# Kernel tuning notes

Hardware: AMD Instinct MI355X
Metric: run time of the kernel (lower is better)

Reference implementation:

```python
import jax, jax.numpy as jnp
import numpy as np

N = 100000
E = 1600000
BN_EPS = 1e-5


def setup_inputs() -> dict:
    key = jax.random.key(0)
    ks = jax.random.split(key, 32)
    rn = lambda k, shape, s=0.05: jax.random.normal(k, shape, jnp.float32) * s
    inp = {
        "x": jax.random.normal(ks[0], (N, 2), jnp.float32),
        "edge_index": jax.random.randint(ks[1], (2, E), 0, N, dtype=jnp.int64),
        # GIN conv1 mlp: Linear(1,256) -> BN(256) -> ReLU -> Linear(256,128)
        "w1": rn(ks[2], (1, 256)), "b1": rn(ks[3], (256,)),
        "g1": jax.random.uniform(ks[4], (256,), jnp.float32, 0.5, 1.5),
        "be1": rn(ks[5], (256,)),
        "m1": rn(ks[6], (256,)),
        "v1": jax.random.uniform(ks[7], (256,), jnp.float32, 0.5, 1.5),
        "w2": rn(ks[8], (256, 128)), "b2": rn(ks[9], (128,)),
        # GIN conv2 mlp: Linear(128,64) -> BN(64) -> ReLU -> Linear(64,64)
        "w3": rn(ks[10], (128, 64)), "b3": rn(ks[11], (64,)),
        "g2": jax.random.uniform(ks[12], (64,), jnp.float32, 0.5, 1.5),
        "be2": rn(ks[13], (64,)),
        "m2": rn(ks[14], (64,)),
        "v2": jax.random.uniform(ks[15], (64,), jnp.float32, 0.5, 1.5),
        # Bilinear(64, 64, 96)
        "wb": rn(ks[16], (96, 64, 64)), "bb": rn(ks[17], (96,)),
        # linear3: 96 -> 6
        "w5": rn(ks[18], (96, 6)), "b5": rn(ks[19], (6,)),
        # linear2: 6 -> 6
        "w6": rn(ks[20], (6, 6)), "b6": rn(ks[21], (6,)),
    }
    return inp


def reference(x, edge_index, w1, b1, g1, be1, m1, v1, w2, b2,
              w3, b3, g2, be2, m2, v2, w4_unused=None, wb=None, bb=None,
              w5=None, b5=None, w6=None, b6=None):
    # note: kept signature explicit below; see _reference
    raise NotImplementedError


def _bn(h, g, b, m, v):
    # inference-mode batchnorm with running stats
    return (h - m) * jax.lax.rsqrt(v + BN_EPS) * g + b


def reference(x, edge_index, w1, b1, g1, be1, m1, v1, w2, b2,
              w3, b3, g2, be2, m2, v2, wb, bb, w5, b5, w6, b6):
    src, dst = edge_index[0], edge_index[1]
    n = x.shape[0]

    def agg(h):
        # GIN sum aggregation: (1+eps)*x + sum_{j in N(i)} x_j, eps=0
        return h + jax.ops.segment_sum(h[src], dst, num_segments=n)

    def block(col):  # col: [n, 1]
        h = agg(col)
        h = jnp.maximum(_bn(h @ w1 + b1, g1, be1, m1, v1), 0.0) @ w2 + b2  # [n,128]
        h = agg(h)
        h = jnp.maximum(_bn(h @ w3 + b3, g2, be2, m2, v2), 0.0)            # mlp2 ends with BN+ReLU? no:
        return h

    # mlp2 = Linear(128,64)->BN(64)->ReLU->Linear(64,64); rebuild correctly inline:
    def block2(col):
        h = agg(col)
        h = jnp.maximum(_bn(h @ w1 + b1, g1, be1, m1, v1), 0.0) @ w2 + b2  # [n,128]
        h = agg(h)
        h = jnp.maximum(_bn(h @ w3 + b3, g2, be2, m2, v2), 0.0)
        return h

    h1 = block2(x[:, 1:2])  # column tmp-1 = 1 first
    h2 = block2(x[:, 0:1])  # then column 0
    # mlp2's final Linear(64,64) is folded below? No -- apply final linear of mlp2:
    # (handled in block2 already via w3 only; second linear uses separate weights)
    hb = jnp.einsum('ni,kij,nj->nk', h1, wb, h2) + bb  # Bilinear(64,64,96)
    h = jnp.maximum(hb @ w5 + b5, 0.0)                 # relu(linear3)
    h = h @ w6 + b6                                    # linear2
    return jax.nn.log_softmax(h, axis=1)
```

## Files before the change

### kernel.cpp

```cpp
#include <hip/hip_runtime.h>
#include <hip/hip_bf16.h>

#define NN 100000
#define NE 1600000
#define EPS 1e-5f
#define NCHUNK 98
#define NB 196
#define BCAP2 10240
#define RND 4096
#define NRND 391

typedef __attribute__((ext_vector_type(8))) short short8;
typedef __attribute__((ext_vector_type(4))) float f32x4;

__device__ __forceinline__ float b2f_lo(unsigned u){ return __uint_as_float(u << 16); }
__device__ __forceinline__ float b2f_hi(unsigned u){ return __uint_as_float(u & 0xffff0000u); }
__device__ __forceinline__ float b2f_u(unsigned short u){ return __uint_as_float(((unsigned)u) << 16); }
__device__ __forceinline__ unsigned short f2b(float f){
  __hip_bfloat16 h = __float2bfloat16(f);
  return __builtin_bit_cast(unsigned short, h);
}

__global__ void k_probe(const int* __restrict__ ei32, int* __restrict__ flag, int* __restrict__ gcur){
  __shared__ int cnt;
  if (threadIdx.x == 0) cnt = 0;
  __syncthreads();
  if (ei32[threadIdx.x * 2 + 1] == 0) atomicAdd(&cnt, 1);
  __syncthreads();
  if (threadIdx.x == 0) flag[0] = (cnt > 200) ? 1 : 0;
  for (int i = threadIdx.x; i < NB; i += 256) gcur[i] = i * BCAP2;
}

__global__ __launch_bounds__(1024) void k_bin(const void* __restrict__ ei, const int* __restrict__ flag,
                                              int* __restrict__ gcur, int* __restrict__ staged){
  __shared__ int hcnt[256];
  __shared__ int pref[256];
  __shared__ int bnd[200];
  __shared__ int hrun[196];
  __shared__ int gb[196];
  __shared__ int sbuf[RND];
  int t = threadIdx.x;
  int base = blockIdx.x * RND;
  bool f64 = (flag[0] != 0);
  int pay[4], bkt[4];
  #pragma unroll
  for (int k = 0; k < 4; ++k){
    int e = base + k * 1024 + t;
    if (e < NE){
      int src, dst;
      if (f64){ src = (int)((const long long*)ei)[e]; dst = (int)((const long long*)ei)[NE + e]; }
      else    { src = ((const int*)ei)[e];            dst = ((const int*)ei)[NE + e]; }
      pay[k] = (src << 9) | (dst & 511);
      bkt[k] = dst >> 9;
    } else { pay[k] = 0; bkt[k] = -1; }
  }
  if (t < 256) hcnt[t] = 0;
  __syncthreads();
  #pragma unroll
  for (int k = 0; k < 4; ++k)
    if (bkt[k] >= 0) atomicAdd(&hcnt[bkt[k]], 1);
  __syncthreads();
  if (t < 256) pref[t] = hcnt[t];
  __syncthreads();
  for (int off = 1; off < 256; off <<= 1){
    int v = 0;
    if (t < 256 && t >= off) v = pref[t - off];
    __syncthreads();
    if (t < 256) pref[t] += v;
    __syncthreads();
  }
  if (t < 196){
    int excl = pref[t] - hcnt[t];
    bnd[t] = excl;
    hrun[t] = excl;
    gb[t] = (hcnt[t] > 0) ? atomicAdd(&gcur[t], hcnt[t]) : 0;
  }
  if (t == 196) bnd[196] = 0;
  __syncthreads();
  if (t == 0) bnd[196] = pref[255];
  __syncthreads();
  #pragma unroll
  for (int k = 0; k < 4; ++k)
    if (bkt[k] >= 0){
      int lp = atomicAdd(&hrun[bkt[k]], 1);
      sbuf[lp] = pay[k];
    }
  __syncthreads();
  int total = bnd[196];
  for (int i = t; i < total; i += 1024){
    int b = 0;
    #pragma unroll
    for (int sh = 128; sh > 0; sh >>= 1)
      if (b + sh <= 196 && bnd[b + sh] <= i) b += sh;
    staged[gb[b] + (i - bnd[b])] = sbuf[i];
  }
}

__global__ __launch_bounds__(256) void k_bdeg(const int* __restrict__ staged, const int* __restrict__ gcur,
                                              int* __restrict__ deg){
  __shared__ int dcnt[512];
  int b = blockIdx.x, t = threadIdx.x;
  for (int l = t; l < 512; l += 256) dcnt[l] = 0;
  __syncthreads();
  int cnt = min(gcur[b] - b * BCAP2, BCAP2);
  const int* sp = staged + b * BCAP2;
  for (int i = t; i < cnt; i += 256)
    atomicAdd(&dcnt[sp[i] & 511], 1);
  __syncthreads();
  for (int l = t; l < 512; l += 256){
    int n = b * 512 + l;
    if (n < NN) deg[n] = dcnt[l];
  }
}

__global__ void k_scan1(const int* __restrict__ deg, int* __restrict__ cinc, int* __restrict__ part){
  __shared__ int b[1024];
  int i = blockIdx.x * 1024 + threadIdx.x;
  int v = (i < NN) ? deg[i] : 0;
  b[threadIdx.x] = v; __syncthreads();
  for (int off = 1; off < 1024; off <<= 1){
    int t = (threadIdx.x >= off) ? b[threadIdx.x - off] : 0;
    __syncthreads();
    b[threadIdx.x] += t;
    __syncthreads();
  }
  if (i < NN) cinc[i] = b[threadIdx.x];
  if (threadIdx.x == 1023) part[blockIdx.x] = b[1023];
}

__global__ void k_scan2(int* __restrict__ part, int nchunk){
  __shared__ int b[128];
  int tid = threadIdx.x;
  int v = (tid < nchunk) ? part[tid] : 0;
  b[tid] = v; __syncthreads();
  for (int off = 1; off < 128; off <<= 1){
    int t = (tid >= off) ? b[tid - off] : 0;
    __syncthreads();
    b[tid] += t;
    __syncthreads();
  }
  if (tid < nchunk) part[tid] = b[tid] - v;
}

__global__ void k_scan3(const int* __restrict__ deg, const int* __restrict__ cinc,
                        const int* __restrict__ part, int* __restrict__ rowp){
  int i = blockIdx.x * 1024 + threadIdx.x;
  if (i < NN){
    rowp[i] = cinc[i] - deg[i] + part[blockIdx.x];
  }
  if (i == 0) rowp[NN] = NE;
}

__global__ __launch_bounds__(256) void k_scatter2(const int* __restrict__ staged, const int* __restrict__ gcur,
                                                  const int* __restrict__ rowp, int* __restrict__ colidx){
  __shared__ int cur[512];
  int b = blockIdx.x, t = threadIdx.x;
  for (int l = t; l < 512; l += 256){
    int n = b * 512 + l;
    cur[l] = (n < NN) ? rowp[n] : 0;
  }
  __syncthreads();
  int cnt = min(gcur[b] - b * BCAP2, BCAP2);
  const int* sp = staged + b * BCAP2;
  for (int i = t; i < cnt; i += 256){
    int p = sp[i];
    int pos = atomicAdd(&cur[p & 511], 1);
    colidx[pos] = p >> 9;
  }
}

__global__ void k_prep_sort(const float* __restrict__ w1, const float* __restrict__ b1,
                            const float* __restrict__ g1, const float* __restrict__ be1,
                            const float* __restrict__ m1, const float* __restrict__ v1,
                            const float* __restrict__ w3, const float* __restrict__ b3,
                            const float* __restrict__ g2, const float* __restrict__ be2,
                            const float* __restrict__ m2, const float* __restrict__ v2,
                            float* __restrict__ aC, float* __restrict__ cC,
                            float* __restrict__ thrS, int* __restrict__ pos,
                            unsigned short* __restrict__ w3s, float* __restrict__ b3p){
  __shared__ float key[256];
  __shared__ int idx[256];
  int tid = threadIdx.x;
  {
    float inv = rsqrtf(v1[tid] + EPS);
    float sc = g1[tid] * inv;
    float a = w1[tid] * sc;
    float c = (b1[tid] - m1[tid]) * sc + be1[tid];
    aC[tid] = a; cC[tid] = c;
    key[tid] = (a != 0.0f) ? (-c / a) : __int_as_float(0x7f800000);
    idx[tid] = tid;
  }
  __syncthreads();
  for (int k = 2; k <= 256; k <<= 1){
    for (int j = k >> 1; j > 0; j >>= 1){
      int ixj = tid ^ j;
      if (ixj > tid){
        float k1 = key[tid], k2 = key[ixj];
        bool asc = ((tid & k) == 0);
        if ((k1 > k2) == asc){
          int i1 = idx[tid];
          key[tid] = k2; key[ixj] = k1;
          idx[tid] = idx[ixj]; idx[ixj] = i1;
        }
      }
      __syncthreads();
    }
  }
  thrS[tid] = key[tid];
  pos[idx[tid]] = tid;
  if (tid < 64){
    float i2 = rsqrtf(v2[tid] + EPS);
    b3p[tid] = (b3[tid] - m2[tid]) * i2 * g2[tid] + be2[tid];
  }
  for (int id = tid; id < 8192; id += 256){
    int cs = id >> 11, r = id & 2047;
    int kt = r >> 9;  r &= 511;
    int l = r >> 3;   int mi = r & 7;
    int krow = kt * 32 + (l >> 4) * 8 + mi;
    int col  = cs * 16 + (l & 15);
    float i2 = rsqrtf(v2[col] + EPS);
    w3s[id] = f2b(w3[krow * 64 + col] * i2 * g2[col]);
  }
}

__global__ void k_tab(const float* __restrict__ aC, const float* __restrict__ cC,
                      const int* __restrict__ pos, const float* __restrict__ w2,
                      const float* __restrict__ b2, unsigned short* __restrict__ tabG){
  __shared__ float ca[256], cc[256];
  int t = blockIdx.x;
  int tid = threadIdx.x;
  {
    float a = aC[tid], c = cC[tid];
    int p = pos[tid];
    bool act = (a > 0.f) ? (p < t) : ((a < 0.f) ? (p >= t) : (c > 0.f));
    ca[tid] = act ? a : 0.f;
    cc[tid] = act ? c : 0.f;
  }
  __syncthreads();
  int f = tid & 127, sel = tid >> 7;
  const float* coef = sel ? cc : ca;
  float acc = sel ? b2[f] : 0.f;
  #pragma unroll 8
  for (int j = 0; j < 256; ++j)
    acc = fmaf(coef[j], w2[j * 128 + f], acc);
  tabG[t * 256 + sel * 128 + f] = f2b(acc);
}

__global__ void k_wbS(const float* __restrict__ wb, unsigned short* __restrict__ wbS){
  int id = blockIdx.x * 256 + threadIdx.x;
  if (id >= 64 * 6144) return;
  int j = id / 6144;
  int r = id % 6144;
  int f = r >> 9;  r &= 511;
  int l = r >> 3;  int mi = r & 7;
  int kt = f / 6, cs = f % 6;
  int i = kt * 32 + (l >> 4) * 8 + mi;
  int k = cs * 16 + (l & 15);
  wbS[id] = f2b(wb[(k * 64 + i) * 64 + j]);
}

__global__ void k_sagg(const float* __restrict__ x, const int* __restrict__ rowp,
                       const int* __restrict__ colidx, const float* __restrict__ thrS,
                       float4* __restrict__ info){
  __shared__ float thr[256];
  thr[threadIdx.x] = thrS[threadIdx.x];
  __syncthreads();
  int n = blockIdx.x * 256 + threadIdx.x;
  if (n >= NN) return;
  float2 xv = ((const float2*)x)[n];
  float sA = xv.y, sB = xv.x;
  int s0 = rowp[n], s1 = rowp[n + 1];
  for (int e = s0; e < s1; ++e){
    int j = colidx[e];
    float2 xj = ((const float2*)x)[j];
    sA += xj.y; sB += xj.x;
  }
  int tA = 0, tB = 0;
  #pragma unroll
  for (int sh = 128; sh > 0; sh >>= 1){
    if (tA + sh <= 256 && thr[tA + sh - 1] < sA) tA += sh;
    if (tB + sh <= 256 && thr[tB + sh - 1] < sB) tB += sh;
  }
  info[n] = make_float4(sA, sB, __uint_as_float((unsigned)tA | ((unsigned)tB << 16)), 0.f);
}

__global__ __launch_bounds__(1024) void k_agg(
    const float4* __restrict__ info, const int* __restrict__ rowp,
    const int* __restrict__ colidx, const unsigned short* __restrict__ tabG,
    unsigned short* __restrict__ mA, unsigned short* __restrict__ mB){
  extern __shared__ unsigned tab32[];
  for (int i = threadIdx.x; i < 257 * 128; i += 1024)
    tab32[i] = ((const unsigned*)tabG)[i];
  __syncthreads();
  int lane = threadIdx.x & 63;
  int wv = (blockIdx.x * 1024 + threadIdx.x) >> 6;
  int nw = (gridDim.x * 1024) >> 6;
  int p  = lane >> 5;
  int fq = lane & 31;
  for (int n = wv; n < NN; n += nw){
    int s0 = rowp[n], cnt = rowp[n + 1] - s0 + 1;
    float a0 = 0.f, a1 = 0.f, a2 = 0.f, a3 = 0.f;
    for (int base = 0; base < cnt; base += 64){
      int nb = base + lane;
      float4 inf;
      if (nb < cnt){
        int j = (nb == 0) ? n : colidx[s0 + nb - 1];
        inf = info[j];
      } else inf = make_float4(0, 0, 0, 0);
      int m = min(cnt - base, 64);
      for (int q = 0; q < m; ++q){
        float sA = __shfl(inf.x, q);
        float sB = __shfl(inf.y, q);
        unsigned tt = __float_as_uint(__shfl(inf.z, q));
        float s = p ? sB : sA;
        int   t = p ? (int)(tt >> 16) : (int)(tt & 0xffffu);
        const unsigned* rp = &tab32[t * 128];
        uint2 av = *(const uint2*)&rp[fq * 2];
        uint2 bv = *(const uint2*)&rp[64 + fq * 2];
        a0 += fmaf(s, b2f_lo(av.x), b2f_lo(bv.x));
        a1 += fmaf(s, b2f_hi(av.x), b2f_hi(bv.x));
        a2 += fmaf(s, b2f_lo(av.y), b2f_lo(bv.y));
        a3 += fmaf(s, b2f_hi(av.y), b2f_hi(bv.y));
      }
    }
    unsigned short* dst = (p ? mB : mA) + n * 128 + fq * 4;
    unsigned o0 = (unsigned)f2b(a0) | ((unsigned)f2b(a1) << 16);
    unsigned o1 = (unsigned)f2b(a2) | ((unsigned)f2b(a3) << 16);
    *((uint2*)dst) = make_uint2(o0, o1);
  }
}

__global__ void k_mlp2(const unsigned short* __restrict__ mA, const unsigned short* __restrict__ mB,
                       const unsigned short* __restrict__ w3s, const float* __restrict__ b3p,
                       unsigned short* __restrict__ h1, unsigned short* __restrict__ h2T){
  int lane = threadIdx.x & 63;
  int tile = (blockIdx.x * blockDim.x + threadIdx.x) >> 6;
  const int NT = 2 * NN / 16;
  if (tile >= NT) return;
  bool pB = (tile >= NN / 16);
  const unsigned short* src = pB ? (mB + (size_t)(tile - NN / 16) * 16 * 128)
                                 : (mA + (size_t)tile * 16 * 128);
  short8 afr[4];
  {
    int row = lane & 15, ko = (lane >> 4) * 8;
    #pragma unroll
    for (int kt = 0; kt < 4; ++kt)
      afr[kt] = *(const short8*)(src + row * 128 + kt * 32 + ko);
  }
  f32x4 acc[4];
  #pragma unroll
  for (int cs = 0; cs < 4; ++cs){
    f32x4 a = {0.f, 0.f, 0.f, 0.f};
    #pragma unroll
    for (int kt = 0; kt < 4; ++kt){
      short8 b = *(const short8*)(w3s + ((cs * 4 + kt) * 64 + lane) * 8);
      a = __builtin_amdgcn_mfma_f32_16x16x32_bf16(afr[kt], b, a, 0, 0, 0);
    }
    acc[cs] = a;
  }
  int col0 = lane & 15, r0 = (lane >> 4) * 4;
  if (!pB){
    int nb = tile * 16;
    #pragma unroll
    for (int cs = 0; cs < 4; ++cs){
      float bias = b3p[cs * 16 + col0];
      #pragma unroll
      for (int r = 0; r < 4; ++r){
        float v = fmaxf(acc[cs][r] + bias, 0.f);
        h1[(size_t)(nb + r0 + r) * 64 + cs * 16 + col0] = f2b(v);
      }
    }
  } else {
    int nb = (tile - NN / 16) * 16;
    #pragma unroll
    for (int cs = 0; cs < 4; ++cs){
      float bias = b3p[cs * 16 + col0];
      unsigned p0 = (unsigned)f2b(fmaxf(acc[cs][0] + bias, 0.f)) | ((unsigned)f2b(fmaxf(acc[cs][1] + bias, 0.f)) << 16);
      unsigned p1 = (unsigned)f2b(fmaxf(acc[cs][2] + bias, 0.f)) | ((unsigned)f2b(fmaxf(acc[cs][3] + bias, 0.f)) << 16);
      *(uint2*)(h2T + (size_t)(cs * 16 + col0) * NN + nb + r0) = make_uint2(p0, p1);
    }
  }
}

__global__ __launch_bounds__(128, 2) void k_bil(
    const unsigned short* __restrict__ h1, const unsigned short* __restrict__ h2T,
    const unsigned short* __restrict__ wbS, const float* __restrict__ bbv,
    const float* __restrict__ w5, const float* __restrict__ b5,
    const float* __restrict__ w6, const float* __restrict__ b6,
    float* __restrict__ out){
  __shared__ unsigned short h2sT[64 * 64];
  __shared__ float red[64 * 96];
  int tid = threadIdx.x;
  int lane = tid & 63;
  int wv = tid >> 6;
  int nb = blockIdx.x * 64;
  int rl = lane & 15, ko = (lane >> 4) * 8;
  for (int i = tid; i < 64 * 64; i += 128){
    int j = i >> 6, l = (i >> 2) & 15, rt = i & 3;
    int n = nb + rt * 16 + l;
    h2sT[i] = (n < NN) ? h2T[(size_t)j * NN + n] : (unsigned short)0;
  }
  float af[4][2][8];
  #pragma unroll
  for (int rt = 0; rt < 4; ++rt){
    int row = nb + rt * 16 + rl;
    #pragma unroll
    for (int kt = 0; kt < 2; ++kt){
      if (row < NN){
        uint4 rv = *(const uint4*)(h1 + (size_t)row * 64 + kt * 32 + ko);
        af[rt][kt][0] = b2f_lo(rv.x); af[rt][kt][1] = b2f_hi(rv.x);
        af[rt][kt][2] = b2f_lo(rv.y); af[rt][kt][3] = b2f_hi(rv.y);
        af[rt][kt][4] = b2f_lo(rv.z); af[rt][kt][5] = b2f_hi(rv.z);
        af[rt][kt][6] = b2f_lo(rv.w); af[rt][kt][7] = b2f_hi(rv.w);
      } else {
        #pragma unroll
        for (int e = 0; e < 8; ++e) af[rt][kt][e] = 0.f;
      }
    }
  }
  __syncthreads();
  f32x4 acc[4][6];
  #pragma unroll
  for (int rt = 0; rt < 4; ++rt)
    #pragma unroll
    for (int cs = 0; cs < 6; ++cs)
      acc[rt][cs] = (f32x4){0.f, 0.f, 0.f, 0.f};
  const unsigned short* wp = wbS + (size_t)lane * 8;
  int j0 = wv * 32, j1 = j0 + 32;
  for (int j = j0; j < j1; ++j){
    uint4 bf[2][6];
    #pragma unroll
    for (int kt = 0; kt < 2; ++kt)
      #pragma unroll
      for (int cs = 0; cs < 6; ++cs)
        bf[kt][cs] = *(const uint4*)(wp + (size_t)(j * 12 + kt * 6 + cs) * 512);
    uint2 hsv = *(const uint2*)(h2sT + j * 64 + rl * 4);
    float hsr[4];
    hsr[0] = b2f_lo(hsv.x); hsr[1] = b2f_hi(hsv.x);
    hsr[2] = b2f_lo(hsv.y); hsr[3] = b2f_hi(hsv.y);
    #pragma unroll
    for (int rt = 0; rt < 4; ++rt){
      float hs = hsr[rt];
      short8 a0, a1;
      #pragma unroll
      for (int e = 0; e < 8; ++e){
        a0[e] = (short)f2b(af[rt][0][e] * hs);
        a1[e] = (short)f2b(af[rt][1][e] * hs);
      }
      #pragma unroll
      for (int cs = 0; cs < 6; ++cs){
        acc[rt][cs] = __builtin_amdgcn_mfma_f32_16x16x32_bf16(a0, __builtin_bit_cast(short8, bf[0][cs]), acc[rt][cs], 0, 0, 0);
        acc[rt][cs] = __builtin_amdgcn_mfma_f32_16x16x32_bf16(a1, __builtin_bit_cast(short8, bf[1][cs]), acc[rt][cs], 0, 0, 0);
      }
    }
  }
  if (wv == 1){
    #pragma unroll
    for (int rt = 0; rt < 4; ++rt)
      #pragma unroll
      for (int cs = 0; cs < 6; ++cs){
        int col = cs * 16 + rl;
        #pragma unroll
        for (int r = 0; r < 4; ++r){
          int row = rt * 16 + (lane >> 4) * 4 + r;
          red[row * 96 + col] = acc[rt][cs][r];
        }
      }
  }
  __syncthreads();
  if (wv == 0){
    #pragma unroll
    for (int rt = 0; rt < 4; ++rt)
      #pragma unroll
      for (int cs = 0; cs < 6; ++cs){
        int col = cs * 16 + rl;
        #pragma unroll
        for (int r = 0; r < 4; ++r){
          int row = rt * 16 + (lane >> 4) * 4 + r;
          acc[rt][cs][r] += red[row * 96 + col];
        }
      }
    unsigned short* hbs = (unsigned short*)red;
    #pragma unroll
    for (int rt = 0; rt < 4; ++rt)
      #pragma unroll
      for (int cs = 0; cs < 6; ++cs){
        int col = cs * 16 + rl;
        float bias = bbv[col];
        #pragma unroll
        for (int r = 0; r < 4; ++r){
          int rowl = rt * 16 + (lane >> 4) * 4 + r;
          hbs[rowl * 98 + col] = f2b(acc[rt][cs][r] + bias);
        }
      }
    int n = nb + lane;
    if (n < NN){
      float u[6];
      #pragma unroll
      for (int q = 0; q < 6; ++q) u[q] = b5[q];
      for (int jj = 0; jj < 96; ++jj){
        float hv = b2f_u(hbs[lane * 98 + jj]);
        #pragma unroll
        for (int q = 0; q < 6; ++q) u[q] = fmaf(hv, w5[jj * 6 + q], u[q]);
      }
      #pragma unroll
      for (int q = 0; q < 6; ++q) u[q] = fmaxf(u[q], 0.f);
      float v[6];
      #pragma unroll
      for (int q = 0; q < 6; ++q){
        float a2 = b6[q];
        #pragma unroll
        for (int pp = 0; pp < 6; ++pp) a2 = fmaf(u[pp], w6[pp * 6 + q], a2);
        v[q] = a2;
      }
      float mx = v[0];
      #pragma unroll
      for (int q = 1; q < 6; ++q) mx = fmaxf(mx, v[q]);
      float se = 0.f;
      #pragma unroll
      for (int q = 0; q < 6; ++q) se += expf(v[q] - mx);
      float ls = logf(se);
      #pragma unroll
      for (int q = 0; q < 6; ++q) out[(size_t)n * 6 + q] = v[q] - mx - ls;
    }
  }
}

extern "C" void kernel_launch(void* const* d_in, const int* in_sizes, int n_in,
                              void* d_out, int out_size, void* d_ws, size_t ws_size,
                              hipStream_t stream){
  const float* x   = (const float*)d_in[0];
  const void*  ei  = d_in[1];
  const float* w1  = (const float*)d_in[2];
  const float* b1  = (const float*)d_in[3];
  const float* g1  = (const float*)d_in[4];
  const float* be1 = (const float*)d_in[5];
  const float* m1  = (const float*)d_in[6];
  const float* v1  = (const float*)d_in[7];
  const float* w2  = (const float*)d_in[8];
  const float* b2  = (const float*)d_in[9];
  const float* w3  = (const float*)d_in[10];
  const float* b3  = (const float*)d_in[11];
  const float* g2  = (const float*)d_in[12];
  const float* be2 = (const float*)d_in[13];
  const float* m2  = (const float*)d_in[14];
  const float* v2  = (const float*)d_in[15];
  const float* wb  = (const float*)d_in[16];
  const float* bb  = (const float*)d_in[17];
  const float* w5  = (const float*)d_in[18];
  const float* b5  = (const float*)d_in[19];
  const float* w6  = (const float*)d_in[20];
  const float* b6  = (const float*)d_in[21];
  float* out = (float*)d_out;

  char* ws = (char*)d_ws;
  size_t off = 0;
  auto alloc = [&](size_t bytes) -> void* {
    void* p = ws + off;
    off += (bytes + 255) & ~(size_t)255;
    return p;
  };
  int* deg      = (int*)alloc((size_t)NN * 4);
  int* rowp     = (int*)alloc((size_t)(NN + 1) * 4);
  int* cinc     = (int*)alloc((size_t)NN * 4);
  int* part     = (int*)alloc(1024 * 4);
  int* flag     = (int*)alloc(256);
  int* gcur     = (int*)alloc((size_t)NB * 4 + 256);
  int* colidx   = (int*)alloc((size_t)NE * 4);
  float4* info  = (float4*)alloc((size_t)NN * 16);
  unsigned short* tabG = (unsigned short*)alloc(257 * 256 * 2);
  float* thrS   = (float*)alloc(256 * 4);
  float* aC     = (float*)alloc(256 * 4);
  float* cC     = (float*)alloc(256 * 4);
  int* pos      = (int*)alloc(256 * 4);
  unsigned short* w3s  = (unsigned short*)alloc(8192 * 2);
  float* b3p    = (float*)alloc(64 * 4);
  unsigned short* wbS  = (unsigned short*)alloc((size_t)393216 * 2);
  unsigned short* mA   = (unsigned short*)alloc((size_t)NN * 128 * 2);
  unsigned short* mB   = (unsigned short*)alloc((size_t)NN * 128 * 2);
  unsigned short* h1   = (unsigned short*)alloc((size_t)NN * 64 * 2);
  unsigned short* h2T  = (unsigned short*)alloc((size_t)NN * 64 * 2);
  int* staged   = (int*)mA;

  k_probe<<<1, 256, 0, stream>>>((const int*)ei, flag, gcur);
  k_bin<<<NRND, 1024, 0, stream>>>(ei, flag, gcur, staged);
  k_bdeg<<<NB, 256, 0, stream>>>(staged, gcur, deg);
  k_scan1<<<NCHUNK, 1024, 0, stream>>>(deg, cinc, part);
  k_scan2<<<1, 128, 0, stream>>>(part, NCHUNK);
  k_scan3<<<NCHUNK, 1024, 0, stream>>>(deg, cinc, part, rowp);
  k_scatter2<<<NB, 256, 0, stream>>>(staged, gcur, rowp, colidx);
  k_prep_sort<<<1, 256, 0, stream>>>(w1, b1, g1, be1, m1, v1, w3, b3, g2, be2, m2, v2,
                                     aC, cC, thrS, pos, w3s, b3p);
  k_tab<<<257, 256, 0, stream>>>(aC, cC, pos, w2, b2, tabG);
  k_wbS<<<(64 * 6144 + 255) / 256, 256, 0, stream>>>(wb, wbS);
  k_sagg<<<(NN + 255) / 256, 256, 0, stream>>>(x, rowp, colidx, thrS, info);
  hipFuncSetAttribute((const void*)k_agg, hipFuncAttributeMaxDynamicSharedMemorySize, 257 * 128 * 4);
  k_agg<<<256, 1024, 257 * 128 * 4, stream>>>(info, rowp, colidx, tabG, mA, mB);
  k_mlp2<<<(2 * NN / 16 + 3) / 4, 256, 0, stream>>>(mA, mB, w3s, b3p, h1, h2T);
  k_bil<<<(NN + 63) / 64, 128, 0, stream>>>(h1, h2T, wbS, bb, w5, b5, w6, b6, out);
}
```

Measured before the change: 336.0 us.

## Restructure bilinear kernel to share double-buffered weight tiles across 8 waves

The bilinear kernel moves from 64-row blocks of 2 waves that split the j reduction to 256-row blocks of 8 waves. Each wave now owns 64 rows and half of the 96 output columns, so the cross-wave reduction through shared memory goes away. Weight tiles for each j are loaded cooperatively into double-buffered LDS with a prefetch of the next j, replacing per-wave redundant global loads. The cost is a __syncthreads every iteration, fewer blocks (391) with one block per CU, and a sequential 64-step j loop per wave.

Result: slower. 359.9 us (+7.1%).

```diff
diff --git a/kernel.cpp b/kernel.cpp
--- a/kernel.cpp
+++ b/kernel.cpp
@@ -382,28 +382,33 @@
   }
 }
 
-__global__ __launch_bounds__(128, 2) void k_bil(
+__global__ __launch_bounds__(512, 1) void k_bil(
     const unsigned short* __restrict__ h1, const unsigned short* __restrict__ h2T,
     const unsigned short* __restrict__ wbS, const float* __restrict__ bbv,
     const float* __restrict__ w5, const float* __restrict__ b5,
     const float* __restrict__ w6, const float* __restrict__ b6,
     float* __restrict__ out){
-  __shared__ unsigned short h2sT[64 * 64];
-  __shared__ float red[64 * 96];
+  __shared__ unsigned short smem[28672];
+  unsigned short* h2sT = smem;
+  unsigned short* bufs = smem + 16384;
   int tid = threadIdx.x;
   int lane = tid & 63;
-  int wv = tid >> 6;
-  int nb = blockIdx.x * 64;
+  int wid = tid >> 6;
+  int kg = wid & 1, rh = wid >> 1;
+  int nb = blockIdx.x * 256;
   int rl = lane & 15, ko = (lane >> 4) * 8;
-  for (int i = tid; i < 64 * 64; i += 128){
-    int j = i >> 6, l = (i >> 2) & 15, rt = i & 3;
-    int n = nb + rt * 16 + l;
-    h2sT[i] = (n < NN) ? h2T[(size_t)j * NN + n] : (unsigned short)0;
+  for (int i = tid; i < 64 * 256; i += 512){
+    int j = i >> 8, r = i & 255;
+    int rh2 = r >> 6, q = r & 63;
+    int rt2 = q >> 4, rl2 = q & 15;
+    int n = nb + r;
+    unsigned short v = (n < NN) ? h2T[(size_t)j * NN + n] : (unsigned short)0;
+    h2sT[j * 256 + rh2 * 64 + rl2 * 4 + rt2] = v;
   }
   float af[4][2][8];
   #pragma unroll
   for (int rt = 0; rt < 4; ++rt){
-    int row = nb + rt * 16 + rl;
+    int row = nb + rh * 64 + rt * 16 + rl;
     #pragma unroll
     for (int kt = 0; kt < 2; ++kt){
       if (row < NN){
@@ -418,23 +423,38 @@
       }
     }
   }
-  __syncthreads();
-  f32x4 acc[4][6];
+  int f1 = wid, f2 = 8 + wid;
+  {
+    uint4 v0 = *(const uint4*)(wbS + ((size_t)(0 * 12 + f1) * 512 + lane * 8));
+    *(uint4*)(bufs + f1 * 512 + lane * 8) = v0;
+    if (wid < 4){
+      uint4 v1 = *(const uint4*)(wbS + ((size_t)(0 * 12 + f2) * 512 + lane * 8));
+      *(uint4*)(bufs + f2 * 512 + lane * 8) = v1;
+    }
+  }
+  __syncthreads();
+  f32x4 acc[4][3];
   #pragma unroll
   for (int rt = 0; rt < 4; ++rt)
     #pragma unroll
-    for (int cs = 0; cs < 6; ++cs)
+    for (int cs = 0; cs < 3; ++cs)
       acc[rt][cs] = (f32x4){0.f, 0.f, 0.f, 0.f};
-  const unsigned short* wp = wbS + (size_t)lane * 8;
-  int j0 = wv * 32, j1 = j0 + 32;
-  for (int j = j0; j < j1; ++j){
-    uint4 bf[2][6];
+  int cur = 0;
+  for (int j = 0; j < 64; ++j){
+    uint4 v0, v1;
+    bool pre = (j + 1 < 64);
+    if (pre){
+      v0 = *(const uint4*)(wbS + ((size_t)((j + 1) * 12 + f1) * 512 + lane * 8));
+      if (wid < 4) v1 = *(const uint4*)(wbS + ((size_t)((j + 1) * 12 + f2) * 512 + lane * 8));
+    }
+    const unsigned short* bp = bufs + cur * 6144;
+    uint4 bf[2][3];
     #pragma unroll
     for (int kt = 0; kt < 2; ++kt)
       #pragma unroll
-      for (int cs = 0; cs < 6; ++cs)
-        bf[kt][cs] = *(const uint4*)(wp + (size_t)(j * 12 + kt * 6 + cs) * 512);
-    uint2 hsv = *(const uint2*)(h2sT + j * 64 + rl * 4);
+      for (int cs = 0; cs < 3; ++cs)
+        bf[kt][cs] = *(const uint4*)(bp + (kt * 6 + kg * 3 + cs) * 512 + lane * 8);
+    uint2 hsv = *(const uint2*)(h2sT + j * 256 + rh * 64 + rl * 4);
     float hsr[4];
     hsr[0] = b2f_lo(hsv.x); hsr[1] = b2f_hi(hsv.x);
     hsr[2] = b2f_lo(hsv.y); hsr[3] = b2f_hi(hsv.y);
@@ -448,58 +468,41 @@
         a1[e] = (short)f2b(af[rt][1][e] * hs);
       }
       #pragma unroll
-      for (int cs = 0; cs < 6; ++cs){
+      for (int cs = 0; cs < 3; ++cs){
         acc[rt][cs] = __builtin_amdgcn_mfma_f32_16x16x32_bf16(a0, __builtin_bit_cast(short8, bf[0][cs]), acc[rt][cs], 0, 0, 0);
         acc[rt][cs] = __builtin_amdgcn_mfma_f32_16x16x32_bf16(a1, __builtin_bit_cast(short8, bf[1][cs]), acc[rt][cs], 0, 0, 0);
       }
     }
-  }
-  if (wv == 1){
-    #pragma unroll
-    for (int rt = 0; rt < 4; ++rt)
-      #pragma unroll
-      for (int cs = 0; cs < 6; ++cs){
-        int col = cs * 16 + rl;
-        #pragma unroll
-        for (int r = 0; r < 4; ++r){
-          int row = rt * 16 + (lane >> 4) * 4 + r;
-          red[row * 96 + col] = acc[rt][cs][r];
-        }
-      }
-  }
-  __syncthreads();
-  if (wv == 0){
-    #pragma unroll
-    for (int rt = 0; rt < 4; ++rt)
-      #pragma unroll
-      for (int cs = 0; cs < 6; ++cs){
-        int col = cs * 16 + rl;
-        #pragma unroll
-        for (int r = 0; r < 4; ++r){
-          int row = rt * 16 + (lane >> 4) * 4 + r;
-          acc[rt][cs][r] += red[row * 96 + col];
-        }
-      }
-    unsigned short* hbs = (unsigned short*)red;
-    #pragma unroll
-    for (int rt = 0; rt < 4; ++rt)
-      #pragma unroll
-      for (int cs = 0; cs < 6; ++cs){
-        int col = cs * 16 + rl;
-        float bias = bbv[col];
-        #pragma unroll
-        for (int r = 0; r < 4; ++r){
-          int rowl = rt * 16 + (lane >> 4) * 4 + r;
-          hbs[rowl * 98 + col] = f2b(acc[rt][cs][r] + bias);
-        }
-      }
-    int n = nb + lane;
+    if (pre){
+      unsigned short* wb_ = bufs + (cur ^ 1) * 6144;
+      *(uint4*)(wb_ + f1 * 512 + lane * 8) = v0;
+      if (wid < 4) *(uint4*)(wb_ + f2 * 512 + lane * 8) = v1;
+    }
+    __syncthreads();
+    cur ^= 1;
+  }
+  unsigned short* hbs = smem;
+  #pragma unroll
+  for (int rt = 0; rt < 4; ++rt)
+    #pragma unroll
+    for (int cs = 0; cs < 3; ++cs){
+      int col = kg * 48 + cs * 16 + rl;
+      float bias = bbv[col];
+      #pragma unroll
+      for (int r = 0; r < 4; ++r){
+        int rowl = rh * 64 + rt * 16 + (lane >> 4) * 4 + r;
+        hbs[rowl * 98 + col] = f2b(acc[rt][cs][r] + bias);
+      }
+    }
+  __syncthreads();
+  if (tid < 256){
+    int n = nb + tid;
     if (n < NN){
       float u[6];
       #pragma unroll
       for (int q = 0; q < 6; ++q) u[q] = b5[q];
       for (int jj = 0; jj < 96; ++jj){
-        float hv = b2f_u(hbs[lane * 98 + jj]);
+        float hv = b2f_u(hbs[tid * 98 + jj]);
         #pragma unroll
         for (int q = 0; q < 6; ++q) u[q] = fmaf(hv, w5[jj * 6 + q], u[q]);
       }
@@ -597,5 +600,5 @@
   hipFuncSetAttribute((const void*)k_agg, hipFuncAttributeMaxDynamicSharedMemorySize, 257 * 128 * 4);
   k_agg<<<256, 1024, 257 * 128 * 4, stream>>>(info, rowp, colidx, tabG, mA, mB);
   k_mlp2<<<(2 * NN / 16 + 3) / 4, 256, 0, stream>>>(mA, mB, w3s, b3p, h1, h2T);
-  k_bil<<<(NN + 63) / 64, 128, 0, stream>>>(h1, h2T, wbS, bb, w5, b5, w6, b6, out);
-}
+  k_bil<<<(NN + 255) / 256, 512, 0, stream>>>(h1, h2T, wbS, bb, w5, b5, w6, b6, out);
+}
```
